# Performance work log

Hardware: AMD Instinct MI355X
Metric: run time of the kernel (lower is better)

Reference implementation:

```python
import jax, jax.numpy as jnp
import numpy as np

NUM_GRAPHS = 128
EPS = 1e-5


def _instance_norm(x, seg, num_seg):
    # Per-graph instance norm over rows grouped by seg (PyG InstanceNorm, affine=False).
    ones = jnp.ones((x.shape[0], 1), x.dtype)
    cnt = jnp.maximum(jax.ops.segment_sum(ones, seg, num_segments=num_seg), 1.0)  # [G,1]
    mean = jax.ops.segment_sum(x, seg, num_segments=num_seg) / cnt               # [G,C]
    xc = x - mean[seg]
    var = jax.ops.segment_sum(xc * xc, seg, num_segments=num_seg) / cnt          # [G,C]
    return xc * jax.lax.rsqrt(var[seg] + EPS)


def setup_inputs() -> dict:
    key = jax.random.key(0)
    ks = jax.random.split(key, 8)
    N, E, H, G = 50000, 800000, 64, NUM_GRAPHS
    emb = jax.random.normal(ks[0], (N, H), dtype=jnp.float32)
    edge_index = jax.random.randint(ks[1], (2, E), 0, N, dtype=jnp.int64)
    batch = jnp.sort(jax.random.randint(ks[2], (N,), 0, G, dtype=jnp.int64))
    s1 = 1.0 / np.sqrt(2 * H)
    s2 = 1.0 / np.sqrt(4 * H)
    s3 = 1.0 / np.sqrt(H)
    return {
        "emb": emb,
        "edge_index": edge_index,
        "batch": batch,
        "W1": jax.random.normal(ks[3], (2 * H, 4 * H), dtype=jnp.float32) * s1,
        "b1": jnp.zeros((4 * H,), jnp.float32),
        "W2": jax.random.normal(ks[4], (4 * H, H), dtype=jnp.float32) * s2,
        "b2": jnp.zeros((H,), jnp.float32),
        "W3": jax.random.normal(ks[5], (H, 1), dtype=jnp.float32) * s3,
        "b3": jnp.zeros((1,), jnp.float32),
    }


def reference(emb, edge_index, batch, W1, b1, W2, b2, W3, b3):
    col, row = edge_index[0], edge_index[1]
    # Gather both endpoint embeddings and concat: [E, 2H]
    f12 = jnp.concatenate([emb[col], emb[row]], axis=-1)
    seg = batch[col]  # graph id per edge
    # MLP([2H, 4H, H, 1]): Linear -> InstanceNorm(batch) -> ReLU (dropout=identity in eval)
    h = jnp.maximum(_instance_norm(f12 @ W1 + b1, seg, NUM_GRAPHS), 0.0)
    h = jnp.maximum(_instance_norm(h @ W2 + b2, seg, NUM_GRAPHS), 0.0)
    att_log_logits = h @ W3 + b3  # [E, 1]
    return att_log_logits
```

## Files before the change

kernel.cpp:

```cpp
#include <hip/hip_runtime.h>
#include <hip/hip_bf16.h>
#include <stdint.h>

#define NG 128
#define EPSI 1e-5f

typedef __attribute__((ext_vector_type(8))) __bf16 bf16x8;
typedef __attribute__((ext_vector_type(4))) float f32x4;
typedef int i32x4 __attribute__((ext_vector_type(4)));
typedef unsigned int u32x4 __attribute__((ext_vector_type(4)));

union ABFrag { bf16x8 v; unsigned short u[8]; uint4 q; };
union U8 { uint4 q; unsigned short u[8]; u32x4 e; };

__device__ __forceinline__ float b2f(unsigned short u){
  union { unsigned int i; float f; } v; v.i = ((unsigned int)u) << 16; return v.f;
}
__device__ __forceinline__ unsigned short f2b(float f){
  union { float f; unsigned int i; } v; v.f = f;
  unsigned int r = v.i + 0x7fffu + ((v.i >> 16) & 1u);
  return (unsigned short)(r >> 16);
}
__device__ __forceinline__ unsigned int pk2(float lo, float hi){
  unsigned int r;
  asm("v_cvt_pk_bf16_f32 %0, %1, %2" : "=v"(r) : "v"(lo), "v"(hi));
  return r;
}
__device__ __forceinline__ int4 ldnt(const int4* p){
  i32x4 v = __builtin_nontemporal_load((const i32x4*)p);
  return make_int4(v.x, v.y, v.z, v.w);
}

__global__ void kprep(const float* __restrict__ emb, const float* __restrict__ W1,
                      const float* __restrict__ W2,
                      const int* __restrict__ ei, const int* __restrict__ batch,
                      unsigned short* __restrict__ embb, unsigned short* __restrict__ WcF,
                      unsigned short* __restrict__ W2F, unsigned int* __restrict__ hist,
                      unsigned int* __restrict__ nodeh, int N, int E){
  __shared__ unsigned int h[NG];
  for (int i = threadIdx.x; i < NG; i += 256) h[i] = 0;
  __syncthreads();
  int idx = blockIdx.x * 256 + threadIdx.x;
  int stride = gridDim.x * 256;
  int embCnt4 = N * 16;
  for (int i = idx; i < embCnt4; i += stride){
    float4 v = *(const float4*)(emb + (size_t)i * 4);
    ushort4 o; o.x = f2b(v.x); o.y = f2b(v.y); o.z = f2b(v.z); o.w = f2b(v.w);
    *(ushort4*)(embb + (size_t)i * 4) = o;
  }
  for (int i = idx; i < 32 * 2 * 64 * 8; i += stride){
    int j = i & 7, lane = (i >> 3) & 63, ks = (i >> 9) & 1, tn = i >> 10;
    int quad = lane >> 4, l15 = lane & 15;
    int k = ks * 32 + quad * 8 + j;
    int n = tn * 16 + l15;
    float wv = (n < 256) ? W1[k * 256 + n] : W1[(k + 64) * 256 + (n - 256)];
    WcF[i] = f2b(wv);
  }
  for (int i = idx; i < 4 * 8 * 64 * 8; i += stride){
    int j = i & 7, lane = (i >> 3) & 63, ks = (i >> 9) & 7, w = i >> 12;
    int quad = lane >> 4, l15 = lane & 15;
    W2F[i] = f2b(W2[(ks * 32 + quad * 8 + j) * 64 + w * 16 + l15]);
  }
  for (int e = idx; e < E; e += stride){
    int cn = ei[e];
    atomicAdd(&h[batch[cn]], 1u);
    atomicAdd(&nodeh[cn], 1u);
  }
  __syncthreads();
  for (int i = threadIdx.x; i < NG; i += 256)
    if (h[i]) atomicAdd(&hist[i], h[i]);
}

__global__ void __launch_bounds__(256) kscan(const unsigned int* __restrict__ nodeh,
                      const unsigned int* __restrict__ hist,
                      const int* __restrict__ batch,
                      unsigned int* __restrict__ ncursor,
                      unsigned int* __restrict__ gmeta, int4* __restrict__ einfo, int N){
  __shared__ unsigned int sh[3];
  __shared__ unsigned int wtot[4];
  int g = blockIdx.x;
  int t = threadIdx.x;
  unsigned int part = 0;
  for (int i = t; i < g; i += 256) part += (hist[i] + 31u) & ~31u;
  #pragma unroll
  for (int d = 1; d < 64; d <<= 1) part += __shfl_xor(part, d);
  if ((t & 63) == 0) wtot[t >> 6] = part;
  if (t == 64 || t == 65){
    int target = g + (t - 64);
    int lo = 0, hi = N;
    while (lo < hi){ int mid = (lo + hi) >> 1; if (batch[mid] < target) lo = mid + 1; else hi = mid; }
    sh[1 + (t - 64)] = lo;
  }
  __syncthreads();
  if (t == 0){
    unsigned int pb = wtot[0] + wtot[1] + wtot[2] + wtot[3];
    sh[0] = pb;
    gmeta[g] = pb;
    if (g == NG - 1) gmeta[NG] = pb + ((hist[g] + 31u) & ~31u);
  }
  __syncthreads();
  unsigned int run = sh[0];
  {
    unsigned int cnt = hist[g];
    unsigned int pe = (cnt + 31u) & ~31u;
    for (unsigned int i = cnt + t; i < pe; i += 256)
      einfo[run + i] = make_int4(0, 0, g, -1);
  }
  int lo = (int)sh[1], hi = (int)sh[2];
  int wid = t >> 6;
  for (int base = lo; base < hi; base += 256){
    int i = base + t;
    unsigned int v = (i < hi) ? nodeh[i] : 0u;
    unsigned int x = v;
    #pragma unroll
    for (int d = 1; d < 64; d <<= 1){
      unsigned int y = __shfl_up(x, d);
      if ((t & 63) >= d) x += y;
    }
    if ((t & 63) == 63) wtot[wid] = x;
    __syncthreads();
    unsigned int woff = 0;
    #pragma unroll
    for (int wb = 0; wb < 4; ++wb) if (wb < wid) woff += wtot[wb];
    if (i < hi) ncursor[i] = run + woff + x - v;
    run += wtot[0] + wtot[1] + wtot[2] + wtot[3];
    __syncthreads();
  }
}

__global__ void kscatter(const int* __restrict__ ei, const int* __restrict__ batch, int E,
                         unsigned int* __restrict__ ncursor, int4* __restrict__ einfo){
  int idx = blockIdx.x * 256 + threadIdx.x;
  for (int e = idx; e < E; e += gridDim.x * 256){
    int cn = ei[e], rn = ei[E + e];
    int g = batch[cn];
    unsigned int p = atomicAdd(&ncursor[cn], 1u);
    einfo[p] = make_int4(cn, rn, g, e);
  }
}

__global__ void __launch_bounds__(256) kgemm1(const unsigned short* __restrict__ embb,
    const unsigned short* __restrict__ WcF, const float* __restrict__ b1,
    unsigned short* __restrict__ PQb, int Nn){
  int wave = threadIdx.x >> 6, lane = threadIdx.x & 63;
  int quad = lane >> 4, l15 = lane & 15;
  int tm = blockIdx.x * 4 + wave;
  int tmmax = (Nn + 15) >> 4;
  if (tm >= tmmax) return;
  int m = tm * 16 + l15; if (m >= Nn) m = Nn - 1;
  ABFrag a0, a1;
  a0.q = *(const uint4*)(embb + (size_t)m * 64 + quad * 8);
  a1.q = *(const uint4*)(embb + (size_t)m * 64 + 32 + quad * 8);
  int rowbase = tm * 16 + quad * 4;
  #pragma unroll 4
  for (int tn = 0; tn < 32; ++tn){
    ABFrag b0, b1f;
    b0.q  = *(const uint4*)(WcF + ((size_t)(tn * 2 + 0) * 64 + lane) * 8);
    b1f.q = *(const uint4*)(WcF + ((size_t)(tn * 2 + 1) * 64 + lane) * 8);
    f32x4 acc = {0.f, 0.f, 0.f, 0.f};
    acc = __builtin_amdgcn_mfma_f32_16x16x32_bf16(a0.v, b0.v, acc, 0, 0, 0);
    acc = __builtin_amdgcn_mfma_f32_16x16x32_bf16(a1.v, b1f.v, acc, 0, 0, 0);
    int col = tn * 16 + l15;
    float bias = (col < 256) ? b1[col] : 0.0f;
    #pragma unroll
    for (int r = 0; r < 4; ++r){
      int rowg = rowbase + r;
      if (rowg < Nn) PQb[(size_t)rowg * 512 + col] = f2b(acc[r] + bias);
    }
  }
}

__global__ void __launch_bounds__(256) kstats1(const unsigned short* __restrict__ PQb,
    const int4* __restrict__ einfo, const int* __restrict__ batch,
    const unsigned int* __restrict__ ncursor, const unsigned int* __restrict__ nodeh,
    float* __restrict__ sum1, float* __restrict__ sq1, int N){
  __shared__ float lsum[4][256];
  __shared__ float lsq[4][256];
  int tid = threadIdx.x;
  for (int i = tid; i < 4 * 256; i += 256){ ((float*)lsum)[i] = 0.f; ((float*)lsq)[i] = 0.f; }
  __syncthreads();
  int base = blockIdx.x * 32;
  int gfirst = batch[base];
  int wid = tid >> 6, lane = tid & 63;
  int c4 = lane * 4;
  float T1[4] = {0.f,0.f,0.f,0.f}, T2[4] = {0.f,0.f,0.f,0.f};
  int curg = -1;
  auto flushT = [&](){
    if (curg >= 0){
      unsigned slot = (unsigned)(curg - gfirst);
      if (slot < 4u){
        #pragma unroll
        for (int t = 0; t < 4; ++t){
          atomicAdd(&lsum[slot][c4 + t], T1[t]);
          atomicAdd(&lsq[slot][c4 + t], T2[t]);
        }
      } else {
        #pragma unroll
        for (int t = 0; t < 4; ++t){
          atomicAdd(&sum1[curg * 256 + c4 + t], T1[t]);
          atomicAdd(&sq1[curg * 256 + c4 + t], T2[t]);
        }
      }
      #pragma unroll
      for (int t = 0; t < 4; ++t){ T1[t] = 0.f; T2[t] = 0.f; }
    }
  };
  for (int i = 0; i < 8; ++i){
    int n = base + wid + i * 4;
    if (n >= N) break;
    int g = batch[n];
    unsigned int cnt = nodeh[n];
    if (g != curg){ flushT(); curg = g; }
    if (!cnt) continue;
    unsigned int start = ncursor[n] - cnt;
    ushort4 pv = *(const ushort4*)(PQb + (size_t)n * 512 + c4);
    float S1[4] = {0.f,0.f,0.f,0.f}, S2[4] = {0.f,0.f,0.f,0.f};
    for (unsigned int jb = 0; jb < cnt; jb += 64){
      int jn = (int)min(64u, cnt - jb);
      int rnv = (lane < jn) ? __builtin_nontemporal_load(&einfo[start + jb + (unsigned)lane].y) : 0;
      #pragma unroll 4
      for (int j = 0; j < jn; ++j){
        int rn = __shfl(rnv, j);
        ushort4 qv = *(const ushort4*)(PQb + (size_t)rn * 512 + 256 + c4);
        float q0 = b2f(qv.x), q1 = b2f(qv.y), q2 = b2f(qv.z), q3 = b2f(qv.w);
        S1[0] += q0; S2[0] = fmaf(q0, q0, S2[0]);
        S1[1] += q1; S2[1] = fmaf(q1, q1, S2[1]);
        S1[2] += q2; S2[2] = fmaf(q2, q2, S2[2]);
        S1[3] += q3; S2[3] = fmaf(q3, q3, S2[3]);
      }
    }
    float fc = (float)cnt;
    float p0 = b2f(pv.x), p1 = b2f(pv.y), p2 = b2f(pv.z), p3 = b2f(pv.w);
    T1[0] += fmaf(fc, p0, S1[0]);  T2[0] += fmaf(fmaf(fc, p0, 2.f * S1[0]), p0, S2[0]);
    T1[1] += fmaf(fc, p1, S1[1]);  T2[1] += fmaf(fmaf(fc, p1, 2.f * S1[1]), p1, S2[1]);
    T1[2] += fmaf(fc, p2, S1[2]);  T2[2] += fmaf(fmaf(fc, p2, 2.f * S1[2]), p2, S2[2]);
    T1[3] += fmaf(fc, p3, S1[3]);  T2[3] += fmaf(fmaf(fc, p3, 2.f * S1[3]), p3, S2[3]);
  }
  flushT();
  __syncthreads();
  for (int i = tid; i < 4 * 256; i += 256){
    int slot = i >> 8, ch = i & 255;
    float vs = lsum[slot][ch], vq = lsq[slot][ch];
    if (vs != 0.f || vq != 0.f){
      int g = gfirst + slot;
      atomicAdd(&sum1[g * 256 + ch], vs);
      atomicAdd(&sq1[g * 256 + ch], vq);
    }
  }
}

__global__ void kfin(const float* __restrict__ sum, const float* __restrict__ sq,
                     const unsigned int* __restrict__ hist,
                     float* __restrict__ meanA, float* __restrict__ rstdA, int C){
  int i = blockIdx.x * blockDim.x + threadIdx.x;
  if (i >= NG * C) return;
  int g = i / C;
  float cnt = fmaxf((float)hist[g], 1.0f);
  float m = sum[i] / cnt;
  float v = sq[i] / cnt - m * m;
  meanA[i] = m;
  rstdA[i] = rsqrtf(fmaxf(v, 0.f) + EPSI);
}

__global__ void __launch_bounds__(256) knorm1(unsigned short* __restrict__ PQb,
    const int* __restrict__ batch, const float* __restrict__ mean1,
    const float* __restrict__ rstd1, int N){
  int idx = blockIdx.x * 256 + threadIdx.x;
  if (idx >= N * 32) return;
  int n = idx >> 5, c8 = (idx & 31) * 8;
  int g = batch[n];
  unsigned short* pp = PQb + (size_t)n * 512 + c8;
  U8 pu; pu.q = *(const uint4*)pp;
  const float* mg = mean1 + g * 256 + c8;
  const float* rg = rstd1 + g * 256 + c8;
  float4 m0 = *(const float4*)mg, m1 = *(const float4*)(mg + 4);
  float4 r0 = *(const float4*)rg, r1 = *(const float4*)(rg + 4);
  U8 o;
  o.q.x = pk2((b2f(pu.u[0]) - m0.x) * r0.x, (b2f(pu.u[1]) - m0.y) * r0.y);
  o.q.y = pk2((b2f(pu.u[2]) - m0.z) * r0.z, (b2f(pu.u[3]) - m0.w) * r0.w);
  o.q.z = pk2((b2f(pu.u[4]) - m1.x) * r1.x, (b2f(pu.u[5]) - m1.y) * r1.y);
  o.q.w = pk2((b2f(pu.u[6]) - m1.z) * r1.z, (b2f(pu.u[7]) - m1.w) * r1.w);
  *(uint4*)pp = o.q;
}

__global__ void __launch_bounds__(256, 5) kmain(const unsigned short* __restrict__ PQb,
    const unsigned short* __restrict__ W2F, const int4* __restrict__ einfo,
    const float* __restrict__ rstd1, const float* __restrict__ b2,
    const unsigned int* __restrict__ hist, const unsigned int* __restrict__ gmeta,
    unsigned short* __restrict__ y2b, float* __restrict__ sum2, float* __restrict__ sq2){
  __shared__ unsigned short Blds[4 * 8 * 64 * 8];
  {
    const uint4* src = (const uint4*)W2F;
    uint4* dst = (uint4*)Blds;
    for (int i = threadIdx.x; i < 2048; i += 256) dst[i] = src[i];
  }
  __syncthreads();
  int wave = threadIdx.x >> 6, lane = threadIdx.x & 63;
  int quad = lane >> 4, l15 = lane & 15;
  float b2v[4];
  #pragma unroll
  for (int cg = 0; cg < 4; ++cg) b2v[cg] = b2[cg * 16 + l15];
  int ntiles = (int)(gmeta[NG] >> 5);
  int nw = gridDim.x * 4;
  for (int t = blockIdx.x * 4 + wave; t < ntiles; t += nw){
    int p0 = t * 32;
    int4 ev0 = ldnt(einfo + p0 + l15);
    int4 ev1 = ldnt(einfo + p0 + 16 + l15);
    int g = __builtin_amdgcn_readfirstlane(ev0.z);
    const unsigned short* pp0 = PQb + (size_t)ev0.x * 512 + quad * 8;
    const unsigned short* qq0 = PQb + (size_t)ev0.y * 512 + 256 + quad * 8;
    const unsigned short* pp1 = PQb + (size_t)ev1.x * 512 + quad * 8;
    const unsigned short* qq1 = PQb + (size_t)ev1.y * 512 + 256 + quad * 8;
    const float* rr = rstd1 + g * 256 + quad * 8;
    f32x4 acc[8];
    #pragma unroll
    for (int i = 0; i < 8; ++i){ acc[i][0]=0.f; acc[i][1]=0.f; acc[i][2]=0.f; acc[i][3]=0.f; }
    #pragma unroll 2
    for (int ks = 0; ks < 8; ++ks){
      U8 pu0, qu0, pu1, qu1;
      pu0.q = *(const uint4*)(pp0 + ks * 32);
      qu0.q = *(const uint4*)(qq0 + ks * 32);
      pu1.q = *(const uint4*)(pp1 + ks * 32);
      qu1.q = *(const uint4*)(qq1 + ks * 32);
      float4 ra = *(const float4*)(rr + ks * 32);
      float4 rb = *(const float4*)(rr + ks * 32 + 4);
      ABFrag a0, a1;
      a0.q.x = pk2(fmaxf(0.f, b2f(pu0.u[0]) + b2f(qu0.u[0]) * ra.x),
                   fmaxf(0.f, b2f(pu0.u[1]) + b2f(qu0.u[1]) * ra.y));
      a0.q.y = pk2(fmaxf(0.f, b2f(pu0.u[2]) + b2f(qu0.u[2]) * ra.z),
                   fmaxf(0.f, b2f(pu0.u[3]) + b2f(qu0.u[3]) * ra.w));
      a0.q.z = pk2(fmaxf(0.f, b2f(pu0.u[4]) + b2f(qu0.u[4]) * rb.x),
                   fmaxf(0.f, b2f(pu0.u[5]) + b2f(qu0.u[5]) * rb.y));
      a0.q.w = pk2(fmaxf(0.f, b2f(pu0.u[6]) + b2f(qu0.u[6]) * rb.z),
                   fmaxf(0.f, b2f(pu0.u[7]) + b2f(qu0.u[7]) * rb.w));
      a1.q.x = pk2(fmaxf(0.f, b2f(pu1.u[0]) + b2f(qu1.u[0]) * ra.x),
                   fmaxf(0.f, b2f(pu1.u[1]) + b2f(qu1.u[1]) * ra.y));
      a1.q.y = pk2(fmaxf(0.f, b2f(pu1.u[2]) + b2f(qu1.u[2]) * ra.z),
                   fmaxf(0.f, b2f(pu1.u[3]) + b2f(qu1.u[3]) * ra.w));
      a1.q.z = pk2(fmaxf(0.f, b2f(pu1.u[4]) + b2f(qu1.u[4]) * rb.x),
                   fmaxf(0.f, b2f(pu1.u[5]) + b2f(qu1.u[5]) * rb.y));
      a1.q.w = pk2(fmaxf(0.f, b2f(pu1.u[6]) + b2f(qu1.u[6]) * rb.z),
                   fmaxf(0.f, b2f(pu1.u[7]) + b2f(qu1.u[7]) * rb.w));
      #pragma unroll
      for (int cg = 0; cg < 4; ++cg){
        ABFrag b;
        b.q = *(const uint4*)&Blds[((cg * 8 + ks) * 64 + lane) * 8];
        acc[cg]     = __builtin_amdgcn_mfma_f32_16x16x32_bf16(a0.v, b.v, acc[cg], 0, 0, 0);
        acc[4 + cg] = __builtin_amdgcn_mfma_f32_16x16x32_bf16(a1.v, b.v, acc[4 + cg], 0, 0, 0);
      }
    }
    #pragma unroll
    for (int sub = 0; sub < 2; ++sub)
      #pragma unroll
      for (int r = 0; r < 4; ++r){
        int el = sub * 16 + quad * 4 + r;
        size_t rowo = (size_t)(p0 + el) * 64 + l15;
        #pragma unroll
        for (int cg = 0; cg < 4; ++cg)
          y2b[rowo + cg * 16] = f2b(acc[sub * 4 + cg][r] + b2v[cg]);
      }
    int nl = (int)gmeta[g] + (int)hist[g] - p0;
    #pragma unroll
    for (int cg = 0; cg < 4; ++cg){
      float s = 0.f, qs = 0.f;
      #pragma unroll
      for (int sub = 0; sub < 2; ++sub)
        #pragma unroll
        for (int r = 0; r < 4; ++r){
          int el = sub * 16 + quad * 4 + r;
          if (el < nl){
            float y = acc[sub * 4 + cg][r] + b2v[cg];
            s += y; qs = fmaf(y, y, qs);
          }
        }
      s  += __shfl_xor(s, 16);  s  += __shfl_xor(s, 32);
      qs += __shfl_xor(qs, 16); qs += __shfl_xor(qs, 32);
      if (quad == 0){
        atomicAdd(&sum2[g * 64 + cg * 16 + l15], s);
        atomicAdd(&sq2[g * 64 + cg * 16 + l15], qs);
      }
    }
  }
}

__global__ void kfinal(const unsigned short* __restrict__ y2b, const int4* __restrict__ einfo,
                       const unsigned int* __restrict__ gmeta,
                       const float* __restrict__ mean2, const float* __restrict__ rstd2,
                       const float* __restrict__ W3, const float* __restrict__ b3,
                       float* __restrict__ out){
  int EP = (int)gmeta[NG];
  int sub = threadIdx.x & 7;
  int c8 = sub * 8;
  float w3r[8];
  #pragma unroll
  for (int t = 0; t < 8; ++t) w3r[t] = W3[c8 + t];
  float b3v = b3[0];
  int step = (gridDim.x * blockDim.x) >> 3;
  for (int i = (blockIdx.x * blockDim.x + threadIdx.x) >> 3; i < EP; i += step){
    int4 ev = ldnt(einfo + i);
    U8 yv; yv.e = __builtin_nontemporal_load((const u32x4*)(y2b + (size_t)i * 64 + c8));
    const float* mg = mean2 + ev.z * 64 + c8;
    const float* rg = rstd2 + ev.z * 64 + c8;
    float4 m0 = *(const float4*)mg, m1 = *(const float4*)(mg + 4);
    float4 r0 = *(const float4*)rg, r1 = *(const float4*)(rg + 4);
    float a = 0.f;
    a += fmaxf(0.f, (b2f(yv.u[0]) - m0.x) * r0.x) * w3r[0];
    a += fmaxf(0.f, (b2f(yv.u[1]) - m0.y) * r0.y) * w3r[1];
    a += fmaxf(0.f, (b2f(yv.u[2]) - m0.z) * r0.z) * w3r[2];
    a += fmaxf(0.f, (b2f(yv.u[3]) - m0.w) * r0.w) * w3r[3];
    a += fmaxf(0.f, (b2f(yv.u[4]) - m1.x) * r1.x) * w3r[4];
    a += fmaxf(0.f, (b2f(yv.u[5]) - m1.y) * r1.y) * w3r[5];
    a += fmaxf(0.f, (b2f(yv.u[6]) - m1.z) * r1.z) * w3r[6];
    a += fmaxf(0.f, (b2f(yv.u[7]) - m1.w) * r1.w) * w3r[7];
    a += __shfl_xor(a, 1);
    a += __shfl_xor(a, 2);
    a += __shfl_xor(a, 4);
    if (sub == 0 && ev.w >= 0) out[ev.w] = a + b3v;
  }
}

extern "C" void kernel_launch(void* const* d_in, const int* in_sizes, int n_in,
                              void* d_out, int out_size, void* d_ws, size_t ws_size,
                              hipStream_t stream){
  const float* emb  = (const float*)d_in[0];
  const int*   ei   = (const int*)d_in[1];
  const int*   batch= (const int*)d_in[2];
  const float* W1   = (const float*)d_in[3];
  const float* b1   = (const float*)d_in[4];
  const float* W2   = (const float*)d_in[5];
  const float* b2   = (const float*)d_in[6];
  const float* W3   = (const float*)d_in[7];
  const float* b3   = (const float*)d_in[8];
  int N = in_sizes[0] / 64;
  int E = in_sizes[1] / 2;
  int EPMAX = E + NG * 32;
  float* out = (float*)d_out;

  char* w = (char*)d_ws;
  size_t off = 0;
  auto nxt = [&](size_t bytes) -> char* {
    char* p = w + off;
    off = (off + bytes + 255) & ~(size_t)255;
    return p;
  };
  unsigned short* embb = (unsigned short*)nxt((size_t)N * 64 * 2);
  unsigned short* WcF  = (unsigned short*)nxt(32 * 2 * 64 * 8 * 2);
  unsigned short* W2F  = (unsigned short*)nxt(4 * 8 * 64 * 8 * 2);
  unsigned short* PQb  = (unsigned short*)nxt((size_t)N * 512 * 2);
  unsigned short* y2b  = (unsigned short*)nxt((size_t)EPMAX * 64 * 2);
  int4* einfo = (int4*)nxt((size_t)EPMAX * 16);
  float* mean1 = (float*)nxt(NG * 256 * 4);
  float* rstd1 = (float*)nxt(NG * 256 * 4);
  float* mean2 = (float*)nxt(NG * 64 * 4);
  float* rstd2 = (float*)nxt(NG * 64 * 4);
  unsigned int* ncursor = (unsigned int*)nxt((size_t)N * 4);
  unsigned int* gmeta   = (unsigned int*)nxt((NG + 1) * 4);
  char* zbase = w + off;
  unsigned int* hist  = (unsigned int*)nxt(NG * 4);
  unsigned int* nodeh = (unsigned int*)nxt((size_t)N * 4);
  float* sum1 = (float*)nxt(NG * 256 * 4);
  float* sq1  = (float*)nxt(NG * 256 * 4);
  float* sum2 = (float*)nxt(NG * 64 * 4);
  float* sq2  = (float*)nxt(NG * 64 * 4);
  size_t zbytes = (size_t)((w + off) - zbase);
  hipMemsetAsync(zbase, 0, zbytes, stream);

  kprep<<<2048, 256, 0, stream>>>(emb, W1, W2, ei, batch, embb, WcF, W2F, hist, nodeh, N, E);
  kscan<<<NG, 256, 0, stream>>>(nodeh, hist, batch, ncursor, gmeta, einfo, N);
  kscatter<<<2048, 256, 0, stream>>>(ei, batch, E, ncursor, einfo);
  {
    int tmmax = (N + 15) / 16;
    kgemm1<<<(tmmax + 3) / 4, 256, 0, stream>>>(embb, WcF, b1, PQb, N);
  }
  kstats1<<<(N + 31) / 32, 256, 0, stream>>>(PQb, einfo, batch, ncursor, nodeh, sum1, sq1, N);
  kfin<<<(NG * 256 + 255) / 256, 256, 0, stream>>>(sum1, sq1, hist, mean1, rstd1, 256);
  knorm1<<<(N * 32 + 255) / 256, 256, 0, stream>>>(PQb, batch, mean1, rstd1, N);
  kmain<<<2048, 256, 0, stream>>>(PQb, W2F, einfo, rstd1, b2, hist, gmeta, y2b, sum2, sq2);
  kfin<<<(NG * 64 + 255) / 256, 256, 0, stream>>>(sum2, sq2, hist, mean2, rstd2, 64);
  kfinal<<<2048, 256, 0, stream>>>(y2b, einfo, gmeta, mean2, rstd2, W3, b3, out);
}
```

Baseline: 487.6 us.

## Split edge info into SoA arrays and compute graph histogram from node degrees

Replaces the int4 per-edge record (cn, rn, g, orig) with separate cn/rn/orig arrays plus a per-32-edge tile graph id. Each consumer now loads only the fields it needs (kstats1 reads only rn, kfinal only orig), which cuts wasted bandwidth on strided int4 loads. The per-edge graph histogram with shared atomics is moved into a new khist kernel that sums node degrees by batch. That removes the batch[cn] gather per edge in kprep and kscatter, at the cost of one extra small launch.

```diff
diff --git a/kernel.cpp b/kernel.cpp
--- a/kernel.cpp
+++ b/kernel.cpp
@@ -7,7 +7,6 @@
 
 typedef __attribute__((ext_vector_type(8))) __bf16 bf16x8;
 typedef __attribute__((ext_vector_type(4))) float f32x4;
-typedef int i32x4 __attribute__((ext_vector_type(4)));
 typedef unsigned int u32x4 __attribute__((ext_vector_type(4)));
 
 union ABFrag { bf16x8 v; unsigned short u[8]; uint4 q; };
@@ -26,20 +25,13 @@
   asm("v_cvt_pk_bf16_f32 %0, %1, %2" : "=v"(r) : "v"(lo), "v"(hi));
   return r;
 }
-__device__ __forceinline__ int4 ldnt(const int4* p){
-  i32x4 v = __builtin_nontemporal_load((const i32x4*)p);
-  return make_int4(v.x, v.y, v.z, v.w);
-}
 
 __global__ void kprep(const float* __restrict__ emb, const float* __restrict__ W1,
                       const float* __restrict__ W2,
-                      const int* __restrict__ ei, const int* __restrict__ batch,
+                      const int* __restrict__ ei,
                       unsigned short* __restrict__ embb, unsigned short* __restrict__ WcF,
-                      unsigned short* __restrict__ W2F, unsigned int* __restrict__ hist,
+                      unsigned short* __restrict__ W2F,
                       unsigned int* __restrict__ nodeh, int N, int E){
-  __shared__ unsigned int h[NG];
-  for (int i = threadIdx.x; i < NG; i += 256) h[i] = 0;
-  __syncthreads();
   int idx = blockIdx.x * 256 + threadIdx.x;
   int stride = gridDim.x * 256;
   int embCnt4 = N * 16;
@@ -61,11 +53,18 @@
     int quad = lane >> 4, l15 = lane & 15;
     W2F[i] = f2b(W2[(ks * 32 + quad * 8 + j) * 64 + w * 16 + l15]);
   }
-  for (int e = idx; e < E; e += stride){
-    int cn = ei[e];
-    atomicAdd(&h[batch[cn]], 1u);
-    atomicAdd(&nodeh[cn], 1u);
-  }
+  for (int e = idx; e < E; e += stride)
+    atomicAdd(&nodeh[ei[e]], 1u);
+}
+
+__global__ void khist(const unsigned int* __restrict__ nodeh, const int* __restrict__ batch,
+                      unsigned int* __restrict__ hist, int N){
+  __shared__ unsigned int h[NG];
+  for (int i = threadIdx.x; i < NG; i += 256) h[i] = 0;
+  __syncthreads();
+  int idx = blockIdx.x * 256 + threadIdx.x;
+  for (int i = idx; i < N; i += gridDim.x * 256)
+    atomicAdd(&h[batch[i]], nodeh[i]);
   __syncthreads();
   for (int i = threadIdx.x; i < NG; i += 256)
     if (h[i]) atomicAdd(&hist[i], h[i]);
@@ -75,7 +74,9 @@
                       const unsigned int* __restrict__ hist,
                       const int* __restrict__ batch,
                       unsigned int* __restrict__ ncursor,
-                      unsigned int* __restrict__ gmeta, int4* __restrict__ einfo, int N){
+                      unsigned int* __restrict__ gmeta,
+                      int* __restrict__ ecn, int* __restrict__ ern,
+                      int* __restrict__ eorig, int* __restrict__ tilegid, int N){
   __shared__ unsigned int sh[3];
   __shared__ unsigned int wtot[4];
   int g = blockIdx.x;
@@ -103,8 +104,11 @@
   {
     unsigned int cnt = hist[g];
     unsigned int pe = (cnt + 31u) & ~31u;
-    for (unsigned int i = cnt + t; i < pe; i += 256)
-      einfo[run + i] = make_int4(0, 0, g, -1);
+    for (unsigned int i = cnt + t; i < pe; i += 256){
+      ecn[run + i] = 0; ern[run + i] = 0; eorig[run + i] = -1;
+    }
+    unsigned int nt = pe >> 5, tb = run >> 5;
+    for (unsigned int i = t; i < nt; i += 256) tilegid[tb + i] = g;
   }
   int lo = (int)sh[1], hi = (int)sh[2];
   int wid = t >> 6;
@@ -128,14 +132,15 @@
   }
 }
 
-__global__ void kscatter(const int* __restrict__ ei, const int* __restrict__ batch, int E,
-                         unsigned int* __restrict__ ncursor, int4* __restrict__ einfo){
+__global__ void kscatter(const int* __restrict__ ei, int E,
+                         unsigned int* __restrict__ ncursor,
+                         int* __restrict__ ecn, int* __restrict__ ern,
+                         int* __restrict__ eorig){
   int idx = blockIdx.x * 256 + threadIdx.x;
   for (int e = idx; e < E; e += gridDim.x * 256){
     int cn = ei[e], rn = ei[E + e];
-    int g = batch[cn];
     unsigned int p = atomicAdd(&ncursor[cn], 1u);
-    einfo[p] = make_int4(cn, rn, g, e);
+    ecn[p] = cn; ern[p] = rn; eorig[p] = e;
   }
 }
 
@@ -171,7 +176,7 @@
 }
 
 __global__ void __launch_bounds__(256) kstats1(const unsigned short* __restrict__ PQb,
-    const int4* __restrict__ einfo, const int* __restrict__ batch,
+    const int* __restrict__ ern, const int* __restrict__ batch,
     const unsigned int* __restrict__ ncursor, const unsigned int* __restrict__ nodeh,
     float* __restrict__ sum1, float* __restrict__ sq1, int N){
   __shared__ float lsum[4][256];
@@ -217,7 +222,7 @@
     float S1[4] = {0.f,0.f,0.f,0.f}, S2[4] = {0.f,0.f,0.f,0.f};
     for (unsigned int jb = 0; jb < cnt; jb += 64){
       int jn = (int)min(64u, cnt - jb);
-      int rnv = (lane < jn) ? __builtin_nontemporal_load(&einfo[start + jb + (unsigned)lane].y) : 0;
+      int rnv = (lane < jn) ? __builtin_nontemporal_load(&ern[start + jb + (unsigned)lane]) : 0;
       #pragma unroll 4
       for (int j = 0; j < jn; ++j){
         int rn = __shfl(rnv, j);
@@ -284,7 +289,9 @@
 }
 
 __global__ void __launch_bounds__(256, 5) kmain(const unsigned short* __restrict__ PQb,
-    const unsigned short* __restrict__ W2F, const int4* __restrict__ einfo,
+    const unsigned short* __restrict__ W2F,
+    const int* __restrict__ ecn, const int* __restrict__ ern,
+    const int* __restrict__ tilegid,
     const float* __restrict__ rstd1, const float* __restrict__ b2,
     const unsigned int* __restrict__ hist, const unsigned int* __restrict__ gmeta,
     unsigned short* __restrict__ y2b, float* __restrict__ sum2, float* __restrict__ sq2){
@@ -304,13 +311,15 @@
   int nw = gridDim.x * 4;
   for (int t = blockIdx.x * 4 + wave; t < ntiles; t += nw){
     int p0 = t * 32;
-    int4 ev0 = ldnt(einfo + p0 + l15);
-    int4 ev1 = ldnt(einfo + p0 + 16 + l15);
-    int g = __builtin_amdgcn_readfirstlane(ev0.z);
-    const unsigned short* pp0 = PQb + (size_t)ev0.x * 512 + quad * 8;
-    const unsigned short* qq0 = PQb + (size_t)ev0.y * 512 + 256 + quad * 8;
-    const unsigned short* pp1 = PQb + (size_t)ev1.x * 512 + quad * 8;
-    const unsigned short* qq1 = PQb + (size_t)ev1.y * 512 + 256 + quad * 8;
+    int g = __builtin_amdgcn_readfirstlane(tilegid[t]);
+    int cn0 = __builtin_nontemporal_load(&ecn[p0 + l15]);
+    int rn0 = __builtin_nontemporal_load(&ern[p0 + l15]);
+    int cn1 = __builtin_nontemporal_load(&ecn[p0 + 16 + l15]);
+    int rn1 = __builtin_nontemporal_load(&ern[p0 + 16 + l15]);
+    const unsigned short* pp0 = PQb + (size_t)cn0 * 512 + quad * 8;
+    const unsigned short* qq0 = PQb + (size_t)rn0 * 512 + 256 + quad * 8;
+    const unsigned short* pp1 = PQb + (size_t)cn1 * 512 + quad * 8;
+    const unsigned short* qq1 = PQb + (size_t)rn1 * 512 + 256 + quad * 8;
     const float* rr = rstd1 + g * 256 + quad * 8;
     f32x4 acc[8];
     #pragma unroll
@@ -383,7 +392,8 @@
   }
 }
 
-__global__ void kfinal(const unsigned short* __restrict__ y2b, const int4* __restrict__ einfo,
+__global__ void kfinal(const unsigned short* __restrict__ y2b,
+                       const int* __restrict__ eorig, const int* __restrict__ tilegid,
                        const unsigned int* __restrict__ gmeta,
                        const float* __restrict__ mean2, const float* __restrict__ rstd2,
                        const float* __restrict__ W3, const float* __restrict__ b3,
@@ -397,10 +407,11 @@
   float b3v = b3[0];
   int step = (gridDim.x * blockDim.x) >> 3;
   for (int i = (blockIdx.x * blockDim.x + threadIdx.x) >> 3; i < EP; i += step){
-    int4 ev = ldnt(einfo + i);
+    int orig = __builtin_nontemporal_load(&eorig[i]);
+    int gz = tilegid[i >> 5];
     U8 yv; yv.e = __builtin_nontemporal_load((const u32x4*)(y2b + (size_t)i * 64 + c8));
-    const float* mg = mean2 + ev.z * 64 + c8;
-    const float* rg = rstd2 + ev.z * 64 + c8;
+    const float* mg = mean2 + gz * 64 + c8;
+    const float* rg = rstd2 + gz * 64 + c8;
     float4 m0 = *(const float4*)mg, m1 = *(const float4*)(mg + 4);
     float4 r0 = *(const float4*)rg, r1 = *(const float4*)(rg + 4);
     float a = 0.f;
@@ -415,7 +426,7 @@
     a += __shfl_xor(a, 1);
     a += __shfl_xor(a, 2);
     a += __shfl_xor(a, 4);
-    if (sub == 0 && ev.w >= 0) out[ev.w] = a + b3v;
+    if (sub == 0 && orig >= 0) out[orig] = a + b3v;
   }
 }
 
@@ -448,7 +459,10 @@
   unsigned short* W2F  = (unsigned short*)nxt(4 * 8 * 64 * 8 * 2);
   unsigned short* PQb  = (unsigned short*)nxt((size_t)N * 512 * 2);
   unsigned short* y2b  = (unsigned short*)nxt((size_t)EPMAX * 64 * 2);
-  int4* einfo = (int4*)nxt((size_t)EPMAX * 16);
+  int* ecn   = (int*)nxt((size_t)EPMAX * 4);
+  int* ern   = (int*)nxt((size_t)EPMAX * 4);
+  int* eorig = (int*)nxt((size_t)EPMAX * 4);
+  int* tilegid = (int*)nxt((size_t)(EPMAX / 32 + 1) * 4);
   float* mean1 = (float*)nxt(NG * 256 * 4);
   float* rstd1 = (float*)nxt(NG * 256 * 4);
   float* mean2 = (float*)nxt(NG * 64 * 4);
@@ -465,17 +479,20 @@
   size_t zbytes = (size_t)((w + off) - zbase);
   hipMemsetAsync(zbase, 0, zbytes, stream);
 
-  kprep<<<2048, 256, 0, stream>>>(emb, W1, W2, ei, batch, embb, WcF, W2F, hist, nodeh, N, E);
-  kscan<<<NG, 256, 0, stream>>>(nodeh, hist, batch, ncursor, gmeta, einfo, N);
-  kscatter<<<2048, 256, 0, stream>>>(ei, batch, E, ncursor, einfo);
+  kprep<<<2048, 256, 0, stream>>>(emb, W1, W2, ei, embb, WcF, W2F, nodeh, N, E);
+  khist<<<64, 256, 0, stream>>>(nodeh, batch, hist, N);
+  kscan<<<NG, 256, 0, stream>>>(nodeh, hist, batch, ncursor, gmeta,
+                                ecn, ern, eorig, tilegid, N);
+  kscatter<<<2048, 256, 0, stream>>>(ei, E, ncursor, ecn, ern, eorig);
   {
     int tmmax = (N + 15) / 16;
     kgemm1<<<(tmmax + 3) / 4, 256, 0, stream>>>(embb, WcF, b1, PQb, N);
   }
-  kstats1<<<(N + 31) / 32, 256, 0, stream>>>(PQb, einfo, batch, ncursor, nodeh, sum1, sq1, N);
+  kstats1<<<(N + 31) / 32, 256, 0, stream>>>(PQb, ern, batch, ncursor, nodeh, sum1, sq1, N);
   kfin<<<(NG * 256 + 255) / 256, 256, 0, stream>>>(sum1, sq1, hist, mean1, rstd1, 256);
   knorm1<<<(N * 32 + 255) / 256, 256, 0, stream>>>(PQb, batch, mean1, rstd1, N);
-  kmain<<<2048, 256, 0, stream>>>(PQb, W2F, einfo, rstd1, b2, hist, gmeta, y2b, sum2, sq2);
+  kmain<<<2048, 256, 0, stream>>>(PQb, W2F, ecn, ern, tilegid, rstd1, b2, hist, gmeta,
+                                  y2b, sum2, sq2);
   kfin<<<(NG * 64 + 255) / 256, 256, 0, stream>>>(sum2, sq2, hist, mean2, rstd2, 64);
-  kfinal<<<2048, 256, 0, stream>>>(y2b, einfo, gmeta, mean2, rstd2, W3, b3, out);
-}
+  kfinal<<<2048, 256, 0, stream>>>(y2b, eorig, tilegid, gmeta, mean2, rstd2, W3, b3, out);
+}
```

Measured after the change: 454.3 us. -6.8%, faster.
